# Performance work log

Measured on AMD Instinct MI355X. Metric: run time of the kernel, lower is better.

The kernel has to match this reference:

```python
import jax, jax.numpy as jnp
import numpy as np


def setup_inputs() -> dict:
    key = jax.random.key(0)
    k1, k2 = jax.random.split(key)
    b, t, f = 64, 2048, 1024
    hidden_decoder = jax.random.normal(k1, (b, f), dtype=jnp.float32)
    hiddens_encoder = jax.random.normal(k2, (b, t, f), dtype=jnp.float32)
    return {"hidden_decoder": hidden_decoder, "hiddens_encoder": hiddens_encoder}


def reference(hidden_decoder, hiddens_encoder):
    # scores[b, t] = <hidden_decoder[b], hiddens_encoder[b, t]>
    # (the original loops over t, computes full bxb matmuls and takes diagonals;
    #  this is the equivalent batched dot product)
    scores = jnp.einsum("bf,btf->bt", hidden_decoder, hiddens_encoder)
    a = jax.nn.softmax(scores, axis=1)  # (b, t)
    # context[b, f] = sum_t a[b, t] * hiddens_encoder[b, t, f]
    context = jnp.einsum("bt,btf->bf", a, hiddens_encoder)
    return context
```

## Files before the change

kernel.cpp:

```cpp
#include <hip/hip_runtime.h>
#include <math.h>


#define BB 64
#define TT 2048
#define FF 1024

__global__ __launch_bounds__(256) void attn_pass1(
    const float* __restrict__ hd, const float* __restrict__ he,
    float* __restrict__ part_ctx, float* __restrict__ part_m,
    float* __restrict__ part_l, int S, int Tc)
{
    const int bid  = blockIdx.x;
    const int b    = bid / S;
    const int s    = bid - b * S;
    const int t0   = s * Tc;
    const int lane = threadIdx.x & 63;
    const int wave = threadIdx.x >> 6;

    const float* hdb = hd + (size_t)b * FF;
    float4 hdv[4];
#pragma unroll
    for (int r = 0; r < 4; ++r)
        hdv[r] = *(const float4*)(hdb + 4 * lane + 256 * r);

    float m = -INFINITY, l = 0.f;
    float4 ctx[4];
#pragma unroll
    for (int r = 0; r < 4; ++r) ctx[r] = make_float4(0.f, 0.f, 0.f, 0.f);

    const float* heb = he + ((size_t)b * TT + t0) * (size_t)FF;

    for (int i = wave; i < Tc; i += 4) {
        const float* het = heb + (size_t)i * FF;
        float4 hev[4];
#pragma unroll
        for (int r = 0; r < 4; ++r)
            hev[r] = *(const float4*)(het + 4 * lane + 256 * r);

        float d = 0.f;
#pragma unroll
        for (int r = 0; r < 4; ++r) {
            d += hdv[r].x * hev[r].x + hdv[r].y * hev[r].y +
                 hdv[r].z * hev[r].z + hdv[r].w * hev[r].w;
        }
#pragma unroll
        for (int off = 32; off >= 1; off >>= 1)
            d += __shfl_xor(d, off, 64);

        const float mn    = fmaxf(m, d);
        const float alpha = __expf(m - mn);
        const float w     = __expf(d - mn);
#pragma unroll
        for (int r = 0; r < 4; ++r) {
            ctx[r].x = ctx[r].x * alpha + w * hev[r].x;
            ctx[r].y = ctx[r].y * alpha + w * hev[r].y;
            ctx[r].z = ctx[r].z * alpha + w * hev[r].z;
            ctx[r].w = ctx[r].w * alpha + w * hev[r].w;
        }
        l = l * alpha + w;
        m = mn;
    }

    __shared__ float sm_ctx[4][FF];
    __shared__ float sm_m[4], sm_l[4];
#pragma unroll
    for (int r = 0; r < 4; ++r)
        *(float4*)&sm_ctx[wave][4 * lane + 256 * r] = ctx[r];
    if (lane == 0) { sm_m[wave] = m; sm_l[wave] = l; }
    __syncthreads();

    const float M  = fmaxf(fmaxf(sm_m[0], sm_m[1]), fmaxf(sm_m[2], sm_m[3]));
    const float e0 = __expf(sm_m[0] - M);
    const float e1 = __expf(sm_m[1] - M);
    const float e2 = __expf(sm_m[2] - M);
    const float e3 = __expf(sm_m[3] - M);

    const int f4 = threadIdx.x * 4;
    const float4 c0 = *(const float4*)&sm_ctx[0][f4];
    const float4 c1 = *(const float4*)&sm_ctx[1][f4];
    const float4 c2 = *(const float4*)&sm_ctx[2][f4];
    const float4 c3 = *(const float4*)&sm_ctx[3][f4];
    float4 o;
    o.x = e0 * c0.x + e1 * c1.x + e2 * c2.x + e3 * c3.x;
    o.y = e0 * c0.y + e1 * c1.y + e2 * c2.y + e3 * c3.y;
    o.z = e0 * c0.z + e1 * c1.z + e2 * c2.z + e3 * c3.z;
    o.w = e0 * c0.w + e1 * c1.w + e2 * c2.w + e3 * c3.w;
    *(float4*)(part_ctx + (size_t)bid * FF + f4) = o;

    if (threadIdx.x == 0) {
        part_m[bid] = M;
        part_l[bid] = e0 * sm_l[0] + e1 * sm_l[1] + e2 * sm_l[2] + e3 * sm_l[3];
    }
}

__global__ __launch_bounds__(256) void attn_pass2(
    const float* __restrict__ part_ctx, const float* __restrict__ part_m,
    const float* __restrict__ part_l, float* __restrict__ out, int S)
{
    const int b = blockIdx.x;

    float M = -INFINITY;
    for (int s = 0; s < S; ++s) M = fmaxf(M, part_m[b * S + s]);
    float L = 0.f;
    for (int s = 0; s < S; ++s)
        L += part_l[b * S + s] * __expf(part_m[b * S + s] - M);

    const int f4 = threadIdx.x * 4;
    float4 acc = make_float4(0.f, 0.f, 0.f, 0.f);
    for (int s = 0; s < S; ++s) {
        const float e  = __expf(part_m[b * S + s] - M);
        const float4 c = *(const float4*)(part_ctx + ((size_t)(b * S + s)) * FF + f4);
        acc.x += e * c.x; acc.y += e * c.y; acc.z += e * c.z; acc.w += e * c.w;
    }
    const float inv = 1.f / L;
    float4 o = make_float4(acc.x * inv, acc.y * inv, acc.z * inv, acc.w * inv);
    *(float4*)(out + (size_t)b * FF + f4) = o;
}

extern "C" void kernel_launch(void* const* d_in, const int* in_sizes, int n_in,
                              void* d_out, int out_size, void* d_ws, size_t ws_size,
                              hipStream_t stream) {
    const float* hd = (const float*)d_in[0];
    const float* he = (const float*)d_in[1];
    float* out = (float*)d_out;

    int S = 32;
    while (S > 1 && (size_t)BB * S * (FF * sizeof(float) + 2 * sizeof(float)) > ws_size)
        S >>= 1;
    const int Tc = TT / S;

    float* part_ctx = (float*)d_ws;
    float* part_m   = part_ctx + (size_t)BB * S * FF;
    float* part_l   = part_m + (size_t)BB * S;

    attn_pass1<<<BB * S, 256, 0, stream>>>(hd, he, part_ctx, part_m, part_l, S, Tc);
    attn_pass2<<<BB, 256, 0, stream>>>(part_ctx, part_m, part_l, out, S);
}
```

Baseline: 700.9 us.

## Double-buffer encoder rows in LDS via async global-to-LDS loads

Pass 1 now stages tiles of four encoder rows into a double-buffered shared-memory array using global_load_lds, prefetching the next tile while the current one is computed. Every wave redundantly computes the dot products for all four rows, and each thread then accumulates its own slice of four features for the context. This removes the per-wave online-softmax states and the final cross-wave merge through shared memory. The cost is a block barrier on every tile, four times the dot-product work and heavier LDS read traffic, plus 32KB of LDS per block, which may limit occupancy.

```diff
diff --git a/kernel.cpp b/kernel.cpp
--- a/kernel.cpp
+++ b/kernel.cpp
@@ -5,6 +5,14 @@
 #define BB 64
 #define TT 2048
 #define FF 1024
+#define RR 4
+
+typedef __attribute__((address_space(1))) const void* gas_ptr;
+typedef __attribute__((address_space(3))) void* las_ptr;
+
+__device__ __forceinline__ void gld_lds16(const float* g, float* l) {
+    __builtin_amdgcn_global_load_lds((gas_ptr)g, (las_ptr)l, 16, 0, 0);
+}
 
 __global__ __launch_bounds__(256) void attn_pass1(
     const float* __restrict__ hd, const float* __restrict__ he,
@@ -17,81 +25,85 @@
     const int t0   = s * Tc;
     const int lane = threadIdx.x & 63;
     const int wave = threadIdx.x >> 6;
+    const int nt   = Tc / RR;
+
+    __shared__ float buf[2][RR * FF];
 
     const float* hdb = hd + (size_t)b * FF;
     float4 hdv[4];
 #pragma unroll
-    for (int r = 0; r < 4; ++r)
-        hdv[r] = *(const float4*)(hdb + 4 * lane + 256 * r);
-
-    float m = -INFINITY, l = 0.f;
-    float4 ctx[4];
-#pragma unroll
-    for (int r = 0; r < 4; ++r) ctx[r] = make_float4(0.f, 0.f, 0.f, 0.f);
+    for (int k = 0; k < 4; ++k)
+        hdv[k] = *(const float4*)(hdb + 4 * lane + 256 * k);
 
     const float* heb = he + ((size_t)b * TT + t0) * (size_t)FF;
 
-    for (int i = wave; i < Tc; i += 4) {
-        const float* het = heb + (size_t)i * FF;
-        float4 hev[4];
+    float m = -INFINITY, l = 0.f;
+    float4 ctx = make_float4(0.f, 0.f, 0.f, 0.f);
+
+    {
+        const float* row = heb + (size_t)wave * FF;
 #pragma unroll
-        for (int r = 0; r < 4; ++r)
-            hev[r] = *(const float4*)(het + 4 * lane + 256 * r);
+        for (int k = 0; k < 4; ++k)
+            gld_lds16(row + k * 256 + lane * 4, &buf[0][wave * FF + k * 256]);
+    }
 
-        float d = 0.f;
+    for (int kt = 0; kt < nt; ++kt) {
+        const int cur = kt & 1;
+        __syncthreads();
+
+        if (kt + 1 < nt) {
+            const float* row = heb + ((size_t)(kt + 1) * RR + wave) * FF;
 #pragma unroll
-        for (int r = 0; r < 4; ++r) {
-            d += hdv[r].x * hev[r].x + hdv[r].y * hev[r].y +
-                 hdv[r].z * hev[r].z + hdv[r].w * hev[r].w;
+            for (int k = 0; k < 4; ++k)
+                gld_lds16(row + k * 256 + lane * 4,
+                          &buf[cur ^ 1][wave * FF + k * 256]);
+        }
+
+        float d[RR];
+#pragma unroll
+        for (int r = 0; r < RR; ++r) {
+            float4 hv[4];
+#pragma unroll
+            for (int k = 0; k < 4; ++k)
+                hv[k] = *(const float4*)&buf[cur][r * FF + 4 * lane + 256 * k];
+            float acc = 0.f;
+#pragma unroll
+            for (int k = 0; k < 4; ++k)
+                acc += hdv[k].x * hv[k].x + hdv[k].y * hv[k].y +
+                       hdv[k].z * hv[k].z + hdv[k].w * hv[k].w;
+            d[r] = acc;
         }
 #pragma unroll
-        for (int off = 32; off >= 1; off >>= 1)
-            d += __shfl_xor(d, off, 64);
+        for (int off = 32; off >= 1; off >>= 1) {
+#pragma unroll
+            for (int r = 0; r < RR; ++r)
+                d[r] += __shfl_xor(d[r], off, 64);
+        }
 
-        const float mn    = fmaxf(m, d);
+        float mn = m;
+#pragma unroll
+        for (int r = 0; r < RR; ++r) mn = fmaxf(mn, d[r]);
         const float alpha = __expf(m - mn);
-        const float w     = __expf(d - mn);
+        float w[RR], wsum = 0.f;
 #pragma unroll
-        for (int r = 0; r < 4; ++r) {
-            ctx[r].x = ctx[r].x * alpha + w * hev[r].x;
-            ctx[r].y = ctx[r].y * alpha + w * hev[r].y;
-            ctx[r].z = ctx[r].z * alpha + w * hev[r].z;
-            ctx[r].w = ctx[r].w * alpha + w * hev[r].w;
+        for (int r = 0; r < RR; ++r) { w[r] = __expf(d[r] - mn); wsum += w[r]; }
+
+        const int f4 = threadIdx.x * 4;
+        float4 a = make_float4(ctx.x * alpha, ctx.y * alpha,
+                               ctx.z * alpha, ctx.w * alpha);
+#pragma unroll
+        for (int r = 0; r < RR; ++r) {
+            const float4 rv = *(const float4*)&buf[cur][r * FF + f4];
+            a.x += w[r] * rv.x; a.y += w[r] * rv.y;
+            a.z += w[r] * rv.z; a.w += w[r] * rv.w;
         }
-        l = l * alpha + w;
+        ctx = a;
+        l = l * alpha + wsum;
         m = mn;
     }
 
-    __shared__ float sm_ctx[4][FF];
-    __shared__ float sm_m[4], sm_l[4];
-#pragma unroll
-    for (int r = 0; r < 4; ++r)
-        *(float4*)&sm_ctx[wave][4 * lane + 256 * r] = ctx[r];
-    if (lane == 0) { sm_m[wave] = m; sm_l[wave] = l; }
-    __syncthreads();
-
-    const float M  = fmaxf(fmaxf(sm_m[0], sm_m[1]), fmaxf(sm_m[2], sm_m[3]));
-    const float e0 = __expf(sm_m[0] - M);
-    const float e1 = __expf(sm_m[1] - M);
-    const float e2 = __expf(sm_m[2] - M);
-    const float e3 = __expf(sm_m[3] - M);
-
-    const int f4 = threadIdx.x * 4;
-    const float4 c0 = *(const float4*)&sm_ctx[0][f4];
-    const float4 c1 = *(const float4*)&sm_ctx[1][f4];
-    const float4 c2 = *(const float4*)&sm_ctx[2][f4];
-    const float4 c3 = *(const float4*)&sm_ctx[3][f4];
-    float4 o;
-    o.x = e0 * c0.x + e1 * c1.x + e2 * c2.x + e3 * c3.x;
-    o.y = e0 * c0.y + e1 * c1.y + e2 * c2.y + e3 * c3.y;
-    o.z = e0 * c0.z + e1 * c1.z + e2 * c2.z + e3 * c3.z;
-    o.w = e0 * c0.w + e1 * c1.w + e2 * c2.w + e3 * c3.w;
-    *(float4*)(part_ctx + (size_t)bid * FF + f4) = o;
-
-    if (threadIdx.x == 0) {
-        part_m[bid] = M;
-        part_l[bid] = e0 * sm_l[0] + e1 * sm_l[1] + e2 * sm_l[2] + e3 * sm_l[3];
-    }
+    *(float4*)(part_ctx + (size_t)bid * FF + threadIdx.x * 4) = ctx;
+    if (threadIdx.x == 0) { part_m[bid] = m; part_l[bid] = l; }
 }
 
 __global__ __launch_bounds__(256) void attn_pass2(
```

Result: no change. 698.4 us (-0.4%).
